# Kernel tuning notes

Hardware: AMD Instinct MI355X
Metric: run time of the kernel (lower is better)

Reference implementation:

```python
import jax, jax.numpy as jnp
import numpy as np
from jax import lax

B, H, W, D_MODEL = 2, 64, 64, 96
EXPAND = 2
D_INNER = EXPAND * D_MODEL  # 192
D_STATE = 16
D_CONV = 3
DT_RANK = -(-D_MODEL // 16)  # 6 ('auto')
K = 2  # num_direction


def diagonal_order(size):
    # faithful to SCANS 'diagonal': main diag, then upper tri row-major, then lower tri
    locs = [i * size + i for i in range(size)]
    for i in range(size):
        for j in range(i + 1, size):
            locs.append(i * size + j)
    for i in range(size):
        for j in range(i):
            locs.append(i * size + j)
    return np.asarray(locs, dtype=np.int32)

_ORDER = diagonal_order(H)               # encode: gather by locs_flat
_INV_ORDER = np.argsort(_ORDER).astype(np.int32)  # decode: gather by argsort(locs_flat)


def setup_inputs():
    key = jax.random.key(0)
    ks = jax.random.split(key, 8)
    s = 0.02
    return {
        "x": jax.random.normal(ks[0], (B, H, W, D_MODEL), jnp.float32),
        "w_in": jax.random.normal(ks[1], (2 * D_INNER, D_MODEL), jnp.float32) * s,
        "conv_w": jax.random.normal(ks[2], (D_INNER, 1, D_CONV, D_CONV), jnp.float32) * 0.1,
        "conv_b": jnp.zeros((D_INNER,), jnp.float32),
        "x_proj_w": jax.random.normal(ks[3], (K, DT_RANK + 2 * D_STATE, D_INNER), jnp.float32) * s,
        "dt_w": jax.random.uniform(ks[4], (K, D_INNER, DT_RANK), jnp.float32, -(DT_RANK ** -0.5), DT_RANK ** -0.5),
        "dt_b": jax.random.uniform(ks[5], (K, D_INNER), jnp.float32, -4.6, -2.3),  # inv-softplus of dt in [~1e-2,1e-1]
        "A_logs": jnp.tile(jnp.log(jnp.arange(1, D_STATE + 1, dtype=jnp.float32))[None, :], (K * D_INNER, 1)),
        "Ds": jnp.ones((K * D_INNER,), jnp.float32),
        "ln_g": jnp.ones((D_INNER,), jnp.float32),
        "ln_b": jnp.zeros((D_INNER,), jnp.float32),
        "w_out": jax.random.normal(ks[6], (D_MODEL, D_INNER), jnp.float32) * s,
    }


def _selective_scan(xs, dts, A, Bs, Cs, Ds2, dt_bias):
    # xs, dts: (B,K,D,L); A: (K,D,N); Bs, Cs: (B,K,N,L); Ds2, dt_bias: (K,D)
    delta = jax.nn.softplus(dts + dt_bias[None, :, :, None])           # (B,K,D,L)
    dA = jnp.exp(jnp.einsum('bkdl,kdn->lbkdn', delta, A))              # (L,B,K,D,N)
    dBu = jnp.einsum('bkdl,bknl,bkdl->lbkdn', delta, Bs, xs)           # (L,B,K,D,N)
    Ct = jnp.transpose(Cs, (3, 0, 1, 2))                               # (L,B,K,N)

    h0 = jnp.zeros(dA.shape[1:], dA.dtype)                             # (B,K,D,N)

    def step(h, inp):
        a, bu, c = inp
        h = a * h + bu
        y = jnp.einsum('bkdn,bkn->bkd', h, c)
        return h, y

    _, ys = lax.scan(step, h0, (dA, dBu, Ct))                          # ys: (L,B,K,D)
    return jnp.transpose(ys, (1, 2, 3, 0)) + Ds2[None, :, :, None] * xs  # (B,K,D,L)


def reference(x, w_in, conv_w, conv_b, x_proj_w, dt_w, dt_b, A_logs, Ds, ln_g, ln_b, w_out):
    Bsz, Hh, Ww, _ = x.shape
    L = Hh * Ww
    order = jnp.asarray(_ORDER)
    inv = jnp.asarray(_INV_ORDER)

    xz = x @ w_in.T                                   # (B,H,W,2*D_INNER)
    xi, z = jnp.split(xz, 2, axis=-1)

    xc = jnp.transpose(xi, (0, 3, 1, 2))              # (B,D,H,W)
    xc = lax.conv_general_dilated(xc, conv_w, (1, 1), 'SAME',
                                  feature_group_count=D_INNER)
    xc = jax.nn.silu(xc + conv_b[None, :, None, None])

    xf = xc.reshape(Bsz, D_INNER, L)
    xs0 = xf[:, :, order]                             # diagonal-scan encode
    xs = jnp.stack([xs0, xs0[:, :, ::-1]], axis=1)    # (B,K,D,L), fwd + reversed

    x_dbl = jnp.einsum('bkdl,kcd->bkcl', xs, x_proj_w)
    dts, Bs, Cs = jnp.split(x_dbl, [DT_RANK, DT_RANK + D_STATE], axis=2)
    dts = jnp.einsum('bkrl,kdr->bkdl', dts, dt_w)

    A = -jnp.exp(A_logs).reshape(K, D_INNER, D_STATE)
    out_y = _selective_scan(xs, dts, A, Bs, Cs, Ds.reshape(K, D_INNER), dt_b)  # (B,K,D,L)

    y = out_y[:, 0] + out_y[:, 1, :, ::-1]            # un-flip reverse direction, merge
    y = y[:, :, inv]                                  # diagonal-scan decode
    y = jnp.transpose(y, (0, 2, 1)).reshape(Bsz, Hh, Ww, D_INNER)

    mu = jnp.mean(y, axis=-1, keepdims=True)
    var = jnp.var(y, axis=-1, keepdims=True)
    y = (y - mu) * lax.rsqrt(var + 1e-5) * ln_g + ln_b  # out_norm (LayerNorm)

    y = y * jax.nn.silu(z)
    return y @ w_out.T
```

## Files before the change

### kernel.cpp

```cpp
#include <hip/hip_runtime.h>
#include <math.h>

#define BB 2
#define DM 96
#define DI 192
#define DST 16
#define DRK 6
#define LL 4096
#define NCH 128
#define CT 32

__device__ __forceinline__ int inv_ord(int i, int j) {
    if (i == j) return i;
    if (j > i)  return 64 + i * 63 - (i * (i - 1)) / 2 + (j - i - 1);
    return 2080 + (i * (i - 1)) / 2 + j;
}

__device__ __forceinline__ float silu_f(float v) {
    return v / (1.f + __expf(-v));
}

__device__ __forceinline__ float softplus_f(float a) {
    return a > 20.f ? a : __logf(1.f + __expf(a));
}

__global__ __launch_bounds__(256) void k_gemm_in(const float* __restrict__ x,
                                                 const float* __restrict__ w_in,
                                                 float* __restrict__ xi,
                                                 float* __restrict__ zs) {
    __shared__ float aT[96][68];
    __shared__ float bT[96][68];
    const int tid = threadIdx.x;
    const int bm = blockIdx.x, bn = blockIdx.y;

    for (int f = tid; f < 64 * 24; f += 256) {
        int mm = f / 24, k4 = f % 24;
        float4 v = *(const float4*)(x + (size_t)(bm * 64 + mm) * 96 + k4 * 4);
        aT[k4 * 4 + 0][mm] = v.x; aT[k4 * 4 + 1][mm] = v.y;
        aT[k4 * 4 + 2][mm] = v.z; aT[k4 * 4 + 3][mm] = v.w;
    }
    for (int f = tid; f < 64 * 24; f += 256) {
        int nn = f / 24, k4 = f % 24;
        float4 v = *(const float4*)(w_in + (size_t)(bn * 64 + nn) * 96 + k4 * 4);
        bT[k4 * 4 + 0][nn] = v.x; bT[k4 * 4 + 1][nn] = v.y;
        bT[k4 * 4 + 2][nn] = v.z; bT[k4 * 4 + 3][nn] = v.w;
    }
    __syncthreads();

    const int tn = tid & 15, tm = tid >> 4;
    float acc[4][4] = {};
#pragma unroll 4
    for (int k = 0; k < 96; ++k) {
        float4 av = *(const float4*)&aT[k][tm * 4];
        float4 bv = *(const float4*)&bT[k][tn * 4];
        acc[0][0] += av.x * bv.x; acc[0][1] += av.x * bv.y; acc[0][2] += av.x * bv.z; acc[0][3] += av.x * bv.w;
        acc[1][0] += av.y * bv.x; acc[1][1] += av.y * bv.y; acc[1][2] += av.y * bv.z; acc[1][3] += av.y * bv.w;
        acc[2][0] += av.z * bv.x; acc[2][1] += av.z * bv.y; acc[2][2] += av.z * bv.z; acc[2][3] += av.z * bv.w;
        acc[3][0] += av.w * bv.x; acc[3][1] += av.w * bv.y; acc[3][2] += av.w * bv.z; acc[3][3] += av.w * bv.w;
    }

#pragma unroll
    for (int i = 0; i < 4; ++i) {
#pragma unroll
        for (int j = 0; j < 4; ++j) {
            int m = bm * 64 + tm * 4 + i;
            int n = bn * 64 + tn * 4 + j;
            float v = acc[i][j];
            if (n < DI) xi[(size_t)m * DI + n] = v;
            else        zs[(size_t)m * DI + (n - DI)] = silu_f(v);
        }
    }
}

__global__ __launch_bounds__(256) void k_conv(const float* __restrict__ xi,
                                              const float* __restrict__ cw,
                                              const float* __restrict__ cb,
                                              float* __restrict__ xs0) {
    int t = blockIdx.x * 256 + threadIdx.x;
    int c4 = t % 48;
    int p = t / 48;
    int b = p >> 12;
    int hw = p & 4095;
    int i = hw >> 6, j = hw & 63;
    int c = c4 * 4;
    float a0 = cb[c], a1 = cb[c + 1], a2 = cb[c + 2], a3 = cb[c + 3];
#pragma unroll
    for (int kh = -1; kh <= 1; ++kh) {
        int i2 = i + kh;
        if (i2 < 0 || i2 > 63) continue;
#pragma unroll
        for (int kw = -1; kw <= 1; ++kw) {
            int j2 = j + kw;
            if (j2 < 0 || j2 > 63) continue;
            float4 v = *(const float4*)(xi + ((size_t)(b << 12) + (i2 << 6) + j2) * DI + c);
            int wi = (kh + 1) * 3 + (kw + 1);
            a0 += v.x * cw[(c + 0) * 9 + wi];
            a1 += v.y * cw[(c + 1) * 9 + wi];
            a2 += v.z * cw[(c + 2) * 9 + wi];
            a3 += v.w * cw[(c + 3) * 9 + wi];
        }
    }
    a0 = silu_f(a0); a1 = silu_f(a1); a2 = silu_f(a2); a3 = silu_f(a3);
    int m = inv_ord(i, j);
    *(float4*)(xs0 + ((size_t)(b << 12) + m) * DI + c) = make_float4(a0, a1, a2, a3);
}

__global__ __launch_bounds__(256) void k_proj5(const float* __restrict__ xs0,
                                               const float* __restrict__ xpw,
                                               float* __restrict__ t) {
    __shared__ float xa[192 * 65];
    const int tid = threadIdx.x;
    const int rowbase = blockIdx.x * 64;
    const int k = blockIdx.y >> 1;
    const int chhalf = blockIdx.y & 1;

    for (int f = tid; f < 64 * 48; f += 256) {
        int r = f / 48, q4 = f % 48;
        float4 v = *(const float4*)(xs0 + (size_t)(rowbase + r) * DI + q4 * 4);
        xa[(q4 * 4 + 0) * 65 + r] = v.x;
        xa[(q4 * 4 + 1) * 65 + r] = v.y;
        xa[(q4 * 4 + 2) * 65 + r] = v.z;
        xa[(q4 * 4 + 3) * 65 + r] = v.w;
    }
    __syncthreads();

    const int w = __builtin_amdgcn_readfirstlane(tid >> 6);
    const int lane = tid & 63;
    const int chbase = chhalf * 19 + w * 5;
    const float* wb = xpw + (size_t)k * 38 * DI;

    float acc[5] = {};
    const float* wr[5];
#pragma unroll
    for (int jj = 0; jj < 5; ++jj) {
        int c = chbase + jj; if (c > 37) c = 37;
        wr[jj] = wb + (size_t)c * DI;
    }
#pragma unroll 4
    for (int q = 0; q < DI; ++q) {
        float xv = xa[q * 65 + lane];
#pragma unroll
        for (int jj = 0; jj < 5; ++jj) acc[jj] += wr[jj][q] * xv;
    }
    __syncthreads();

    float* tt = xa;
#pragma unroll
    for (int jj = 0; jj < 5; ++jj) {
        int cl = w * 5 + jj;
        tt[cl * 65 + lane] = acc[jj];
    }
    __syncthreads();
    for (int f = tid; f < 64 * 19; f += 256) {
        int m = f / 19, cl = f % 19;
        int c = chhalf * 19 + cl;
        float v = tt[cl * 65 + m];
        int outc = (k == 0) ? (c < 6 ? 64 + c : c - 6)
                            : (c < 6 ? 70 + c : 26 + c);
        t[(size_t)(rowbase + m) * 80 + outc] = v;
    }
}

__global__ __launch_bounds__(256) void k_scan_a(const float* __restrict__ xs0,
                                                const float* __restrict__ t,
                                                const float* __restrict__ A_logs,
                                                const float* __restrict__ dtw,
                                                const float* __restrict__ dtb,
                                                float* __restrict__ aprod,
                                                float* __restrict__ hend) {
    __shared__ float ld_delta[CT][64];
    __shared__ float ld_dx[CT][64];
    __shared__ float ld_B[CT][16];
    const int tid = threadIdx.x;
    int blk = blockIdx.x;
    int c = blk & (NCH - 1);
    int rest = blk >> 7;
    int dthird = rest % 3;
    int bk = rest / 3;
    int b = bk >> 1, k = bk & 1;
    const int koffB = k ? 32 : 0;
    const int doff = 64 + 6 * k;

    if (tid < 128) {
        int r = tid >> 2, q = tid & 3;
        int gl = c * CT + r;
        int msrc = k ? (LL - 1 - gl) : gl;
        size_t rb = (size_t)(b << 12) + msrc;
        float4 v = *(const float4*)(t + rb * 80 + koffB + q * 4);
        *(float4*)&ld_B[r][q * 4] = v;
    }
    {
        int dloc = tid & 63;
        int d = dthird * 64 + dloc;
        const float* dwr = dtw + ((size_t)k * DI + d) * 6;
        float w0 = dwr[0], w1 = dwr[1], w2 = dwr[2];
        float w3 = dwr[3], w4 = dwr[4], w5 = dwr[5];
        float bias = dtb[k * DI + d];
        for (int f = tid; f < CT * 64; f += 256) {
            int r = f >> 6;
            int gl = c * CT + r;
            int msrc = k ? (LL - 1 - gl) : gl;
            size_t rb = (size_t)(b << 12) + msrc;
            const float* tr = t + rb * 80 + doff;
            float acc = bias + tr[0] * w0 + tr[1] * w1 + tr[2] * w2
                             + tr[3] * w3 + tr[4] * w4 + tr[5] * w5;
            float dl = softplus_f(acc);
            ld_delta[r][dloc] = dl;
            ld_dx[r][dloc] = dl * xs0[rb * DI + d];
        }
    }
    __syncthreads();

    const int dd = tid >> 2, ng = tid & 3;
    const int d = dthird * 64 + dd;
    float Av0, Av1, Av2, Av3;
    {
        const float* ar = A_logs + ((size_t)k * DI + d) * 16 + ng * 4;
        Av0 = -__expf(ar[0]); Av1 = -__expf(ar[1]);
        Av2 = -__expf(ar[2]); Av3 = -__expf(ar[3]);
    }
    float h0 = 0, h1 = 0, h2 = 0, h3 = 0;
    float S = 0.f;
#pragma unroll 4
    for (int l = 0; l < CT; ++l) {
        float dl = ld_delta[l][dd];
        float dx = ld_dx[l][dd];
        float4 bv = *(const float4*)&ld_B[l][ng * 4];
        float a0 = __expf(dl * Av0), a1 = __expf(dl * Av1);
        float a2 = __expf(dl * Av2), a3 = __expf(dl * Av3);
        h0 = a0 * h0 + dx * bv.x; h1 = a1 * h1 + dx * bv.y;
        h2 = a2 * h2 + dx * bv.z; h3 = a3 * h3 + dx * bv.w;
        S += dl;
    }
    float p0 = __expf(Av0 * S), p1 = __expf(Av1 * S);
    float p2 = __expf(Av2 * S), p3 = __expf(Av3 * S);
    size_t o = ((size_t)bk * NCH + c) * 3072 + (size_t)d * 16 + ng * 4;
    *(float4*)(aprod + o) = make_float4(p0, p1, p2, p3);
    *(float4*)(hend + o)  = make_float4(h0, h1, h2, h3);
}

__global__ __launch_bounds__(256) void k_scan_b(const float* __restrict__ aprod,
                                                const float* __restrict__ hend,
                                                float* __restrict__ hinitT) {
    __shared__ float la[128][17];
    __shared__ float lh[128][17];
    const int tid = threadIdx.x;
    int bk = blockIdx.x / 192;
    int rg = blockIdx.x - bk * 192;
    size_t abase = (size_t)bk * NCH * 3072 + rg * 16;

    for (int f = tid; f < 128 * 16; f += 256) {
        int c = f >> 4, r = f & 15;
        la[c][r] = aprod[abase + (size_t)c * 3072 + r];
        lh[c][r] = hend [abase + (size_t)c * 3072 + r];
    }
    __syncthreads();

    const int w = tid >> 6, lane = tid & 63;
    size_t obase = ((size_t)bk * 3072 + rg * 16) * 128;
    for (int rr = w; rr < 16; rr += 4) {
        float a0 = la[lane][rr],      h0 = lh[lane][rr];
        float a1 = la[lane + 64][rr], h1 = lh[lane + 64][rr];
#pragma unroll
        for (int off = 1; off < 64; off <<= 1) {
            float ap = __shfl_up(a0, off), hp = __shfl_up(h0, off);
            if (lane >= off) { h0 = fmaf(a0, hp, h0); a0 *= ap; }
        }
        float he = __shfl_up(h0, 1);
        float hT = __shfl(h0, 63);
        if (lane == 0) he = 0.f;
        hinitT[obase + (size_t)rr * 128 + lane] = he;
#pragma unroll
        for (int off = 1; off < 64; off <<= 1) {
            float ap = __shfl_up(a1, off), hp = __shfl_up(h1, off);
            if (lane >= off) { h1 = fmaf(a1, hp, h1); a1 *= ap; }
        }
        float ae2 = __shfl_up(a1, 1), he2 = __shfl_up(h1, 1);
        if (lane == 0) { ae2 = 1.f; he2 = 0.f; }
        hinitT[obase + (size_t)rr * 128 + 64 + lane] = fmaf(ae2, hT, he2);
    }
}

__global__ __launch_bounds__(256) void k_scan_c(const float* __restrict__ xs0,
                                                const float* __restrict__ t,
                                                const float* __restrict__ A_logs,
                                                const float* __restrict__ dtw,
                                                const float* __restrict__ dtb,
                                                const float* __restrict__ hinitT,
                                                float* __restrict__ ya,
                                                float* __restrict__ yb) {
    __shared__ float ld_delta[CT][64];
    __shared__ float ld_dx[CT][64];
    __shared__ float ld_B[CT][16];
    __shared__ float ld_C[CT][16];
    const int tid = threadIdx.x;
    int blk = blockIdx.x;
    int c = blk & (NCH - 1);
    int rest = blk >> 7;
    int dthird = rest % 3;
    int bk = rest / 3;
    int b = bk >> 1, k = bk & 1;
    const int koffB = k ? 32 : 0;
    const int doff = 64 + 6 * k;

    {
        int r = tid >> 3, q = tid & 7;
        int gl = c * CT + r;
        int msrc = k ? (LL - 1 - gl) : gl;
        size_t rb = (size_t)(b << 12) + msrc;
        float4 v = *(const float4*)(t + rb * 80 + koffB + q * 4);
        if (q < 4) *(float4*)&ld_B[r][q * 4] = v;
        else       *(float4*)&ld_C[r][(q - 4) * 4] = v;
    }
    {
        int dloc = tid & 63;
        int d = dthird * 64 + dloc;
        const float* dwr = dtw + ((size_t)k * DI + d) * 6;
        float w0 = dwr[0], w1 = dwr[1], w2 = dwr[2];
        float w3 = dwr[3], w4 = dwr[4], w5 = dwr[5];
        float bias = dtb[k * DI + d];
        for (int f = tid; f < CT * 64; f += 256) {
            int r = f >> 6;
            int gl = c * CT + r;
            int msrc = k ? (LL - 1 - gl) : gl;
            size_t rb = (size_t)(b << 12) + msrc;
            const float* tr = t + rb * 80 + doff;
            float acc = bias + tr[0] * w0 + tr[1] * w1 + tr[2] * w2
                             + tr[3] * w3 + tr[4] * w4 + tr[5] * w5;
            float dl = softplus_f(acc);
            ld_delta[r][dloc] = dl;
            ld_dx[r][dloc] = dl * xs0[rb * DI + d];
        }
    }
    __syncthreads();

    const int dd = tid >> 2, ng = tid & 3;
    const int d = dthird * 64 + dd;
    float Av0, Av1, Av2, Av3;
    {
        const float* ar = A_logs + ((size_t)k * DI + d) * 16 + ng * 4;
        Av0 = -__expf(ar[0]); Av1 = -__expf(ar[1]);
        Av2 = -__expf(ar[2]); Av3 = -__expf(ar[3]);
    }
    float h0, h1, h2, h3;
    {
        size_t o = ((size_t)bk * 3072 + (size_t)d * 16 + ng * 4) * 128 + c;
        h0 = hinitT[o];
        h1 = hinitT[o + 128];
        h2 = hinitT[o + 256];
        h3 = hinitT[o + 384];
    }
    float* ydst = k ? yb : ya;
    const size_t bbase = (size_t)(b << 12);
#pragma unroll 4
    for (int l = 0; l < CT; ++l) {
        float dl = ld_delta[l][dd];
        float dx = ld_dx[l][dd];
        float4 bv = *(const float4*)&ld_B[l][ng * 4];
        float4 cv = *(const float4*)&ld_C[l][ng * 4];
        float a0 = __expf(dl * Av0), a1 = __expf(dl * Av1);
        float a2 = __expf(dl * Av2), a3 = __expf(dl * Av3);
        h0 = a0 * h0 + dx * bv.x; h1 = a1 * h1 + dx * bv.y;
        h2 = a2 * h2 + dx * bv.z; h3 = a3 * h3 + dx * bv.w;
        float p = h0 * cv.x + h1 * cv.y + h2 * cv.z + h3 * cv.w;
        p += __shfl_xor(p, 1);
        p += __shfl_xor(p, 2);
        if (ng == 0) {
            int gl = c * CT + l;
            int msrc = k ? (LL - 1 - gl) : gl;
            ydst[(bbase + msrc) * DI + d] = p;
        }
    }
}

__global__ __launch_bounds__(256) void k_out(const float* __restrict__ ya,
                                             const float* __restrict__ yb,
                                             const float* __restrict__ xs0,
                                             const float* __restrict__ Ds,
                                             const float* __restrict__ zs,
                                             const float* __restrict__ ln_g,
                                             const float* __restrict__ ln_b,
                                             const float* __restrict__ w_out,
                                             float* __restrict__ out) {
    __shared__ float lnb[16][200];
    __shared__ float bT[96][104];
    __shared__ float stat[16][2];
    const int tid = threadIdx.x;
    const int pb = blockIdx.x * 16;

    for (int f = tid; f < 16 * 48; f += 256) {
        int r = f / 48, q4 = f % 48;
        int p = pb + r;
        int b = p >> 12, pp = p & 4095;
        int m = inv_ord(pp >> 6, pp & 63);
        size_t rbase = ((size_t)(b << 12) + m) * DI + q4 * 4;
        float4 va = *(const float4*)(ya + rbase);
        float4 vb = *(const float4*)(yb + rbase);
        float4 vx = *(const float4*)(xs0 + rbase);
        float4 d0 = *(const float4*)(Ds + q4 * 4);
        float4 d1 = *(const float4*)(Ds + DI + q4 * 4);
        lnb[r][q4 * 4 + 0] = va.x + vb.x + (d0.x + d1.x) * vx.x;
        lnb[r][q4 * 4 + 1] = va.y + vb.y + (d0.y + d1.y) * vx.y;
        lnb[r][q4 * 4 + 2] = va.z + vb.z + (d0.z + d1.z) * vx.z;
        lnb[r][q4 * 4 + 3] = va.w + vb.w + (d0.w + d1.w) * vx.w;
    }
    __syncthreads();

    if (tid < 128) {
        int r = tid >> 3, sub = tid & 7;
        float s = 0.f, s2 = 0.f;
        for (int q = 0; q < 24; ++q) {
            float v = lnb[r][sub * 24 + q];
            s += v; s2 += v * v;
        }
#pragma unroll
        for (int off = 1; off < 8; off <<= 1) {
            s += __shfl_xor(s, off);
            s2 += __shfl_xor(s2, off);
        }
        if (sub == 0) {
            float mu = s * (1.f / 192.f);
            float var = s2 * (1.f / 192.f) - mu * mu;
            stat[r][0] = mu;
            stat[r][1] = rsqrtf(var + 1e-5f);
        }
    }
    __syncthreads();

    for (int f = tid; f < 16 * 48; f += 256) {
        int r = f / 48, q4 = f % 48;
        int p = pb + r;
        float4 vz = *(const float4*)(zs + (size_t)p * DI + q4 * 4);
        float4 g  = *(const float4*)(ln_g + q4 * 4);
        float4 bb = *(const float4*)(ln_b + q4 * 4);
        float mu = stat[r][0], isd = stat[r][1];
        lnb[r][q4*4+0] = ((lnb[r][q4*4+0] - mu) * isd * g.x + bb.x) * vz.x;
        lnb[r][q4*4+1] = ((lnb[r][q4*4+1] - mu) * isd * g.y + bb.y) * vz.y;
        lnb[r][q4*4+2] = ((lnb[r][q4*4+2] - mu) * isd * g.z + bb.z) * vz.z;
        lnb[r][q4*4+3] = ((lnb[r][q4*4+3] - mu) * isd * g.w + bb.w) * vz.w;
    }

    const int tn = tid & 15, tm = tid >> 4;
    float acc[6] = {};
#pragma unroll
    for (int kt = 0; kt < 2; ++kt) {
        __syncthreads();
        for (int f = tid; f < 96 * 24; f += 256) {
            int nn = f / 24, k4 = f % 24;
            float4 v = *(const float4*)(w_out + (size_t)nn * DI + kt * 96 + k4 * 4);
            bT[k4 * 4 + 0][nn] = v.x; bT[k4 * 4 + 1][nn] = v.y;
            bT[k4 * 4 + 2][nn] = v.z; bT[k4 * 4 + 3][nn] = v.w;
        }
        __syncthreads();
#pragma unroll 4
        for (int kq = 0; kq < 96; ++kq) {
            float av = lnb[tm][kt * 96 + kq];
            float2 b0 = *(const float2*)&bT[kq][tn * 6];
            float2 b1 = *(const float2*)&bT[kq][tn * 6 + 2];
            float2 b2 = *(const float2*)&bT[kq][tn * 6 + 4];
            acc[0] += av * b0.x; acc[1] += av * b0.y;
            acc[2] += av * b1.x; acc[3] += av * b1.y;
            acc[4] += av * b2.x; acc[5] += av * b2.y;
        }
    }
    int p = pb + tm;
#pragma unroll
    for (int j = 0; j < 6; ++j)
        out[(size_t)p * DM + tn * 6 + j] = acc[j];
}

extern "C" void kernel_launch(void* const* d_in, const int* in_sizes, int n_in,
                              void* d_out, int out_size, void* d_ws, size_t ws_size,
                              hipStream_t stream) {
    (void)in_sizes; (void)n_in; (void)out_size; (void)ws_size;
    const float* x      = (const float*)d_in[0];
    const float* w_in   = (const float*)d_in[1];
    const float* conv_w = (const float*)d_in[2];
    const float* conv_b = (const float*)d_in[3];
    const float* xpw    = (const float*)d_in[4];
    const float* dtw    = (const float*)d_in[5];
    const float* dtb    = (const float*)d_in[6];
    const float* A_logs = (const float*)d_in[7];
    const float* Ds     = (const float*)d_in[8];
    const float* ln_g   = (const float*)d_in[9];
    const float* ln_b   = (const float*)d_in[10];
    const float* w_out  = (const float*)d_in[11];
    float* out = (float*)d_out;

    float* ws    = (float*)d_ws;
    float* xi    = ws;
    float* zs    = xi + 1572864;
    float* xs0   = zs + 1572864;
    float* tbuf  = xs0 + 1572864;
    float* aprod = tbuf + 1048576;
    float* hend  = aprod + 1572864;
    float* hinitT= hend + 1572864;
    float* ya    = hinitT + 1572864;
    float* yb    = ya + 1572864;

    k_gemm_in<<<dim3(128, 6), 256, 0, stream>>>(x, w_in, xi, zs);
    k_conv<<<1536, 256, 0, stream>>>(xi, conv_w, conv_b, xs0);
    k_proj5<<<dim3(128, 4), 256, 0, stream>>>(xs0, xpw, tbuf);
    k_scan_a<<<4 * 3 * NCH, 256, 0, stream>>>(xs0, tbuf, A_logs, dtw, dtb, aprod, hend);
    k_scan_b<<<4 * 192, 256, 0, stream>>>(aprod, hend, hinitT);
    k_scan_c<<<4 * 3 * NCH, 256, 0, stream>>>(xs0, tbuf, A_logs, dtw, dtb, hinitT, ya, yb);
    k_out<<<512, 256, 0, stream>>>(ya, yb, xs0, Ds, zs, ln_g, ln_b, w_out, out);
}
```

Baseline: 130.8 us.

## Shrink GEMM tiles, split K staging in proj, raise scan unroll, pad LN buffer

The input GEMM now uses 64x32 output tiles with K split into two 48-wide shared-memory stages. This doubles the grid and cuts per-block LDS, and it writes float4 outputs with a block-uniform xi/zs branch. The x-projection kernel stages its 192-wide input in two 96-column halves, halving its LDS footprint to allow more resident blocks. The scan loops are unrolled by 8 instead of 4, and the LayerNorm staging row is padded from 200 to 204 floats, which changes LDS bank mapping. The cost is extra synchronisation, and the larger unroll may raise register pressure.

```diff
diff --git a/kernel.cpp b/kernel.cpp
--- a/kernel.cpp
+++ b/kernel.cpp
@@ -24,50 +24,58 @@
     return a > 20.f ? a : __logf(1.f + __expf(a));
 }
 
-__global__ __launch_bounds__(256) void k_gemm_in(const float* __restrict__ x,
-                                                 const float* __restrict__ w_in,
-                                                 float* __restrict__ xi,
-                                                 float* __restrict__ zs) {
-    __shared__ float aT[96][68];
-    __shared__ float bT[96][68];
+__global__ __launch_bounds__(256) void k_gemm_in2(const float* __restrict__ x,
+                                                  const float* __restrict__ w_in,
+                                                  float* __restrict__ xi,
+                                                  float* __restrict__ zs) {
+    __shared__ float aT[48][68];
+    __shared__ float bT[48][36];
     const int tid = threadIdx.x;
     const int bm = blockIdx.x, bn = blockIdx.y;
-
-    for (int f = tid; f < 64 * 24; f += 256) {
-        int mm = f / 24, k4 = f % 24;
-        float4 v = *(const float4*)(x + (size_t)(bm * 64 + mm) * 96 + k4 * 4);
-        aT[k4 * 4 + 0][mm] = v.x; aT[k4 * 4 + 1][mm] = v.y;
-        aT[k4 * 4 + 2][mm] = v.z; aT[k4 * 4 + 3][mm] = v.w;
-    }
-    for (int f = tid; f < 64 * 24; f += 256) {
-        int nn = f / 24, k4 = f % 24;
-        float4 v = *(const float4*)(w_in + (size_t)(bn * 64 + nn) * 96 + k4 * 4);
-        bT[k4 * 4 + 0][nn] = v.x; bT[k4 * 4 + 1][nn] = v.y;
-        bT[k4 * 4 + 2][nn] = v.z; bT[k4 * 4 + 3][nn] = v.w;
-    }
-    __syncthreads();
-
-    const int tn = tid & 15, tm = tid >> 4;
-    float acc[4][4] = {};
+    const int tn = tid & 7, tm = tid >> 3;
+
+    float acc[2][4] = {};
+#pragma unroll
+    for (int kt = 0; kt < 2; ++kt) {
+        __syncthreads();
+        for (int f = tid; f < 64 * 12; f += 256) {
+            int mm = f / 12, k4 = f % 12;
+            float4 v = *(const float4*)(x + (size_t)(bm * 64 + mm) * 96 + kt * 48 + k4 * 4);
+            aT[k4 * 4 + 0][mm] = v.x; aT[k4 * 4 + 1][mm] = v.y;
+            aT[k4 * 4 + 2][mm] = v.z; aT[k4 * 4 + 3][mm] = v.w;
+        }
+        for (int f = tid; f < 32 * 12; f += 256) {
+            int nn = f / 12, k4 = f % 12;
+            float4 v = *(const float4*)(w_in + (size_t)(bn * 32 + nn) * 96 + kt * 48 + k4 * 4);
+            bT[k4 * 4 + 0][nn] = v.x; bT[k4 * 4 + 1][nn] = v.y;
+            bT[k4 * 4 + 2][nn] = v.z; bT[k4 * 4 + 3][nn] = v.w;
+        }
+        __syncthreads();
 #pragma unroll 4
-    for (int k = 0; k < 96; ++k) {
-        float4 av = *(const float4*)&aT[k][tm * 4];
-        float4 bv = *(const float4*)&bT[k][tn * 4];
-        acc[0][0] += av.x * bv.x; acc[0][1] += av.x * bv.y; acc[0][2] += av.x * bv.z; acc[0][3] += av.x * bv.w;
-        acc[1][0] += av.y * bv.x; acc[1][1] += av.y * bv.y; acc[1][2] += av.y * bv.z; acc[1][3] += av.y * bv.w;
-        acc[2][0] += av.z * bv.x; acc[2][1] += av.z * bv.y; acc[2][2] += av.z * bv.z; acc[2][3] += av.z * bv.w;
-        acc[3][0] += av.w * bv.x; acc[3][1] += av.w * bv.y; acc[3][2] += av.w * bv.z; acc[3][3] += av.w * bv.w;
-    }
-
-#pragma unroll
-    for (int i = 0; i < 4; ++i) {
-#pragma unroll
-        for (int j = 0; j < 4; ++j) {
-            int m = bm * 64 + tm * 4 + i;
-            int n = bn * 64 + tn * 4 + j;
-            float v = acc[i][j];
-            if (n < DI) xi[(size_t)m * DI + n] = v;
-            else        zs[(size_t)m * DI + (n - DI)] = silu_f(v);
+        for (int k = 0; k < 48; ++k) {
+            float2 av = *(const float2*)&aT[k][tm * 2];
+            float4 bv = *(const float4*)&bT[k][tn * 4];
+            acc[0][0] += av.x * bv.x; acc[0][1] += av.x * bv.y;
+            acc[0][2] += av.x * bv.z; acc[0][3] += av.x * bv.w;
+            acc[1][0] += av.y * bv.x; acc[1][1] += av.y * bv.y;
+            acc[1][2] += av.y * bv.z; acc[1][3] += av.y * bv.w;
+        }
+    }
+
+    if (bn < 6) {
+#pragma unroll
+        for (int i = 0; i < 2; ++i) {
+            int m = bm * 64 + tm * 2 + i;
+            *(float4*)(xi + (size_t)m * DI + bn * 32 + tn * 4) =
+                make_float4(acc[i][0], acc[i][1], acc[i][2], acc[i][3]);
+        }
+    } else {
+#pragma unroll
+        for (int i = 0; i < 2; ++i) {
+            int m = bm * 64 + tm * 2 + i;
+            *(float4*)(zs + (size_t)m * DI + (bn - 6) * 32 + tn * 4) =
+                make_float4(silu_f(acc[i][0]), silu_f(acc[i][1]),
+                            silu_f(acc[i][2]), silu_f(acc[i][3]));
         }
     }
 }
@@ -105,25 +113,15 @@
     *(float4*)(xs0 + ((size_t)(b << 12) + m) * DI + c) = make_float4(a0, a1, a2, a3);
 }
 
-__global__ __launch_bounds__(256) void k_proj5(const float* __restrict__ xs0,
+__global__ __launch_bounds__(256) void k_proj6(const float* __restrict__ xs0,
                                                const float* __restrict__ xpw,
                                                float* __restrict__ t) {
-    __shared__ float xa[192 * 65];
+    __shared__ float xa[96 * 65];
     const int tid = threadIdx.x;
     const int rowbase = blockIdx.x * 64;
     const int k = blockIdx.y >> 1;
     const int chhalf = blockIdx.y & 1;
 
-    for (int f = tid; f < 64 * 48; f += 256) {
-        int r = f / 48, q4 = f % 48;
-        float4 v = *(const float4*)(xs0 + (size_t)(rowbase + r) * DI + q4 * 4);
-        xa[(q4 * 4 + 0) * 65 + r] = v.x;
-        xa[(q4 * 4 + 1) * 65 + r] = v.y;
-        xa[(q4 * 4 + 2) * 65 + r] = v.z;
-        xa[(q4 * 4 + 3) * 65 + r] = v.w;
-    }
-    __syncthreads();
-
     const int w = __builtin_amdgcn_readfirstlane(tid >> 6);
     const int lane = tid & 63;
     const int chbase = chhalf * 19 + w * 5;
@@ -136,11 +134,33 @@
         int c = chbase + jj; if (c > 37) c = 37;
         wr[jj] = wb + (size_t)c * DI;
     }
+
+#pragma unroll
+    for (int kh = 0; kh < 2; ++kh) {
+        __syncthreads();
+        for (int f = tid; f < 64 * 24; f += 256) {
+            int r = f / 24, q4 = f % 24;
+            float4 v = *(const float4*)(xs0 + (size_t)(rowbase + r) * DI + kh * 96 + q4 * 4);
+            xa[(q4 * 4 + 0) * 65 + r] = v.x;
+            xa[(q4 * 4 + 1) * 65 + r] = v.y;
+            xa[(q4 * 4 + 2) * 65 + r] = v.z;
+            xa[(q4 * 4 + 3) * 65 + r] = v.w;
+        }
+        __syncthreads();
+        const float* wk0 = wr[0] + kh * 96;
+        const float* wk1 = wr[1] + kh * 96;
+        const float* wk2 = wr[2] + kh * 96;
+        const float* wk3 = wr[3] + kh * 96;
+        const float* wk4 = wr[4] + kh * 96;
 #pragma unroll 4
-    for (int q = 0; q < DI; ++q) {
-        float xv = xa[q * 65 + lane];
-#pragma unroll
-        for (int jj = 0; jj < 5; ++jj) acc[jj] += wr[jj][q] * xv;
+        for (int q = 0; q < 96; ++q) {
+            float xv = xa[q * 65 + lane];
+            acc[0] += wk0[q] * xv;
+            acc[1] += wk1[q] * xv;
+            acc[2] += wk2[q] * xv;
+            acc[3] += wk3[q] * xv;
+            acc[4] += wk4[q] * xv;
+        }
     }
     __syncthreads();
 
@@ -221,7 +241,7 @@
     }
     float h0 = 0, h1 = 0, h2 = 0, h3 = 0;
     float S = 0.f;
-#pragma unroll 4
+#pragma unroll 8
     for (int l = 0; l < CT; ++l) {
         float dl = ld_delta[l][dd];
         float dx = ld_dx[l][dd];
@@ -352,7 +372,7 @@
     }
     float* ydst = k ? yb : ya;
     const size_t bbase = (size_t)(b << 12);
-#pragma unroll 4
+#pragma unroll 8
     for (int l = 0; l < CT; ++l) {
         float dl = ld_delta[l][dd];
         float dx = ld_dx[l][dd];
@@ -382,7 +402,7 @@
                                              const float* __restrict__ ln_b,
                                              const float* __restrict__ w_out,
                                              float* __restrict__ out) {
-    __shared__ float lnb[16][200];
+    __shared__ float lnb[16][204];
     __shared__ float bT[96][104];
     __shared__ float stat[16][2];
     const int tid = threadIdx.x;
@@ -498,9 +518,9 @@
     float* ya    = hinitT + 1572864;
     float* yb    = ya + 1572864;
 
-    k_gemm_in<<<dim3(128, 6), 256, 0, stream>>>(x, w_in, xi, zs);
+    k_gemm_in2<<<dim3(128, 12), 256, 0, stream>>>(x, w_in, xi, zs);
     k_conv<<<1536, 256, 0, stream>>>(xi, conv_w, conv_b, xs0);
-    k_proj5<<<dim3(128, 4), 256, 0, stream>>>(xs0, xpw, tbuf);
+    k_proj6<<<dim3(128, 4), 256, 0, stream>>>(xs0, xpw, tbuf);
     k_scan_a<<<4 * 3 * NCH, 256, 0, stream>>>(xs0, tbuf, A_logs, dtw, dtb, aprod, hend);
     k_scan_b<<<4 * 192, 256, 0, stream>>>(aprod, hend, hinitT);
     k_scan_c<<<4 * 3 * NCH, 256, 0, stream>>>(xs0, tbuf, A_logs, dtw, dtb, hinitT, ya, yb);
```

Measured after the change: 132.0 us. Within noise of the previous version (+0.9%).
